# Optimization experiments

Measured on AMD Instinct MI355X. Metric: run time of the kernel, lower is better.

## Reference

```python
import jax, jax.numpy as jnp
from jax import lax
import numpy as np

# ITA requantization params (from init_kwargs)
MQ, SQ = 16384, 8
MK, SK = 16384, 8
MV, SV = 16384, 8
MA, SA = 5, 12
MAV, SAV = 1, 8
MO, SO = 256, 7
NUM_HEADS = 6


def requantize(x, mult, shift, add=0):
    # x * mult, floor-div by 2**shift, add, clamp to int8 range (values kept in float32)
    return jnp.clip(jnp.floor(x * mult / (2.0 ** shift)) + add, -128.0, 127.0)


def ita_softmax(x):
    # x: [B, h, S, Skv] float32 with integer values in [-128, 127]
    B, h, S, Skv = x.shape
    width, bits = 16, 8
    eps_max = 32.0 * bits / (2 ** bits)  # range_scale * bits / 2**bits = 1.0
    groups = Skv // width
    x3 = x.reshape(B * h, S, Skv).astype(jnp.int32)
    # [groups, BH, S, width] for streaming scan over key chunks
    chunks = x3.reshape(B * h, S, groups, width).transpose(2, 0, 1, 3)

    def step(carry, chunk):
        exp_partial_sum, global_max = carry
        current_max = chunk.max(axis=-1)
        update = current_max > global_max
        max_shift = jnp.floor((current_max - global_max).astype(jnp.float32) * eps_max + 0.5).astype(jnp.int32)
        shift_sum = jnp.where(update, max_shift, 0)
        global_max = jnp.where(update, current_max, global_max)
        diff = global_max[..., None] - chunk  # >= 0
        shift = jnp.floor(diff.astype(jnp.float32) * eps_max + 0.5).astype(jnp.int32)
        # 2**bits >> shift  (256 >> shift; any shift >= 9 yields 0, clamp to keep shift defined)
        exp_sum = jnp.sum(jnp.right_shift(jnp.int32(256), jnp.minimum(shift, 31)), axis=-1).astype(jnp.int32)
        exp_partial_sum = jnp.right_shift(exp_partial_sum, jnp.minimum(shift_sum, 31)) + exp_sum
        return (exp_partial_sum, global_max), None

    init = (jnp.zeros((B * h, S), jnp.int32), jnp.full((B * h, S), -128, jnp.int32))
    (exp_partial_sum, global_max), _ = lax.scan(step, init, chunks)

    # (2**bits - 1) * 2**bits = 65280
    inv = jnp.floor(65280.0 / exp_partial_sum.astype(jnp.float32)).astype(jnp.int32)
    diff = global_max[..., None] - x3  # >= 0
    shift = jnp.floor(diff.astype(jnp.float32) * eps_max + 0.5).astype(jnp.int32)
    res = jnp.right_shift(inv[..., None], jnp.minimum(shift, 31)).astype(jnp.uint8)
    return res.reshape(B, h, S, Skv)


def setup_inputs() -> dict:
    key = jax.random.key(0)
    ks = jax.random.split(key, 9)
    B, N, D = 4, 2048, 384
    scale = 1.0 / np.sqrt(D)
    return {
        "x": jax.random.normal(ks[0], (B, N, D), jnp.float32),
        "wq": jax.random.normal(ks[1], (D, D), jnp.float32) * scale,
        "bq": jnp.zeros((D,), jnp.float32),
        "wk": jax.random.normal(ks[2], (D, D), jnp.float32) * scale,
        "bk": jnp.zeros((D,), jnp.float32),
        "wv": jax.random.normal(ks[3], (D, D), jnp.float32) * scale,
        "bv": jnp.zeros((D,), jnp.float32),
        "wo": jax.random.normal(ks[4], (D, D), jnp.float32) * scale,
        "bo": jnp.zeros((D,), jnp.float32),
        "H": 64,
        "W": 32,
    }


def reference(x, wq, bq, wk, bk, wv, bv, wo, bo, H, W):
    B, N, _ = x.shape
    h = NUM_HEADS
    hd = wq.shape[0] // h

    Q = requantize(x @ wq.T + bq, MQ, SQ)
    K = requantize(x @ wk.T + bk, MK, SK)
    V = requantize(x @ wv.T + bv, MV, SV)

    Qr = Q.reshape(B, N, h, hd).transpose(0, 2, 1, 3)  # [B,h,N,hd]
    Kr = K.reshape(B, N, h, hd).transpose(0, 2, 1, 3)
    Vr = V.reshape(B, N, h, hd).transpose(0, 2, 1, 3)

    logits = requantize(jnp.einsum('bhqd,bhkd->bhqk', Qr, Kr), MA, SA)
    attn = ita_softmax(logits)  # uint8 [B,h,N,N]
    ctx = requantize(jnp.einsum('bhqk,bhkd->bhqd', attn.astype(jnp.float32), Vr), MAV, SAV)
    ctx = ctx.transpose(0, 2, 1, 3).reshape(B, N, h * hd)
    out = requantize(ctx @ wo.T + bo, MO, SO)
    return out
```

## Files before the change

kernel.cpp:

```cpp
#include <hip/hip_runtime.h>
#include <stdint.h>

#define NB 4
#define NN 2048
#define ND 384
#define NH 6
#define HD 64
#define ROWS (NB * NN)

typedef int v4i __attribute__((ext_vector_type(4)));
typedef float v4f __attribute__((ext_vector_type(4)));
typedef float v2f __attribute__((ext_vector_type(2)));
typedef _Float16 half_t;
typedef half_t v8h __attribute__((ext_vector_type(8)));

#define PK_FMA_LO(accv, ap, bp)                                            \
    asm("v_pk_fma_f32 %0, %1, %2, %0 op_sel:[0,0,0] op_sel_hi:[0,1,1]"     \
        : "+v"(accv) : "v"(ap), "v"(bp))
#define PK_FMA_HI(accv, ap, bp)                                            \
    asm("v_pk_fma_f32 %0, %1, %2, %0 op_sel:[1,0,0] op_sel_hi:[1,1,1]"     \
        : "+v"(accv) : "v"(ap), "v"(bp))

__global__ __launch_bounds__(256, 3) void qkv_gemm_kernel(
    const float* __restrict__ X,
    const float* __restrict__ Wq, const float* __restrict__ Wk, const float* __restrict__ Wv,
    const float* __restrict__ Bq, const float* __restrict__ Bk, const float* __restrict__ Bv,
    int8_t* __restrict__ Q8, int8_t* __restrict__ K8, int8_t* __restrict__ V8T,
    int* __restrict__ CS)
{
    __shared__ __attribute__((aligned(16))) float As[2][16][132];
    __shared__ __attribute__((aligned(16))) float Bs[2][16][100];
    __shared__ int lcol[96];

    const int t = threadIdx.x;
    const int tx = t & 15;
    const int ty = t >> 4;
    const int row0 = blockIdx.x * 128;
    const int m = blockIdx.y >> 2;
    const int cl0 = (blockIdx.y & 3) * 96;
    const float* W = (m == 0) ? Wq : (m == 1) ? Wk : Wv;
    const float* Bi = (m == 0) ? Bq : (m == 1) ? Bk : Bv;

    const int sr = t >> 1;
    const int sk = (t & 1) * 8;
    const float* xp = X + (size_t)(row0 + sr) * ND + sk;
    const float* wp = W + (size_t)(cl0 + sr) * ND + sk;

    v2f acc[8][3];
#pragma unroll
    for (int i = 0; i < 8; ++i)
#pragma unroll
        for (int p = 0; p < 3; ++p) acc[i][p] = (v2f)0.0f;

    float4 xa0 = *(const float4*)xp;
    float4 xa1 = *(const float4*)(xp + 4);
    float4 wb0, wb1;
    if (t < 192) { wb0 = *(const float4*)wp; wb1 = *(const float4*)(wp + 4); }

    int cur = 0;
    for (int k0 = 0; k0 < ND; k0 += 16) {
        As[cur][sk + 0][sr] = xa0.x; As[cur][sk + 1][sr] = xa0.y;
        As[cur][sk + 2][sr] = xa0.z; As[cur][sk + 3][sr] = xa0.w;
        As[cur][sk + 4][sr] = xa1.x; As[cur][sk + 5][sr] = xa1.y;
        As[cur][sk + 6][sr] = xa1.z; As[cur][sk + 7][sr] = xa1.w;
        if (t < 192) {
            Bs[cur][sk + 0][sr] = wb0.x; Bs[cur][sk + 1][sr] = wb0.y;
            Bs[cur][sk + 2][sr] = wb0.z; Bs[cur][sk + 3][sr] = wb0.w;
            Bs[cur][sk + 4][sr] = wb1.x; Bs[cur][sk + 5][sr] = wb1.y;
            Bs[cur][sk + 6][sr] = wb1.z; Bs[cur][sk + 7][sr] = wb1.w;
        }

        if (k0 + 16 < ND) {
            xa0 = *(const float4*)(xp + k0 + 16);
            xa1 = *(const float4*)(xp + k0 + 20);
            if (t < 192) {
                wb0 = *(const float4*)(wp + k0 + 16);
                wb1 = *(const float4*)(wp + k0 + 20);
            }
        }
        __syncthreads();

#pragma unroll
        for (int kk = 0; kk < 16; ++kk) {
            const v2f* arp  = (const v2f*)&As[cur][kk][ty * 8];
            const v2f* brp  = (const v2f*)&Bs[cur][kk][tx * 4];
            const v2f* brp2 = (const v2f*)&Bs[cur][kk][64 + tx * 2];
            v2f ap0 = arp[0], ap1 = arp[1], ap2 = arp[2], ap3 = arp[3];
            v2f bp0 = brp[0], bp1 = brp[1], bp2 = brp2[0];

            PK_FMA_LO(acc[0][0], ap0, bp0); PK_FMA_LO(acc[0][1], ap0, bp1);
            PK_FMA_LO(acc[0][2], ap0, bp2);
            PK_FMA_HI(acc[1][0], ap0, bp0); PK_FMA_HI(acc[1][1], ap0, bp1);
            PK_FMA_HI(acc[1][2], ap0, bp2);

            PK_FMA_LO(acc[2][0], ap1, bp0); PK_FMA_LO(acc[2][1], ap1, bp1);
            PK_FMA_LO(acc[2][2], ap1, bp2);
            PK_FMA_HI(acc[3][0], ap1, bp0); PK_FMA_HI(acc[3][1], ap1, bp1);
            PK_FMA_HI(acc[3][2], ap1, bp2);

            PK_FMA_LO(acc[4][0], ap2, bp0); PK_FMA_LO(acc[4][1], ap2, bp1);
            PK_FMA_LO(acc[4][2], ap2, bp2);
            PK_FMA_HI(acc[5][0], ap2, bp0); PK_FMA_HI(acc[5][1], ap2, bp1);
            PK_FMA_HI(acc[5][2], ap2, bp2);

            PK_FMA_LO(acc[6][0], ap3, bp0); PK_FMA_LO(acc[6][1], ap3, bp1);
            PK_FMA_LO(acc[6][2], ap3, bp2);
            PK_FMA_HI(acc[7][0], ap3, bp0); PK_FMA_HI(acc[7][1], ap3, bp1);
            PK_FMA_HI(acc[7][2], ap3, bp2);
        }
        cur ^= 1;
    }

    const int bidx = row0 >> 11;
    const int n0 = row0 & 2047;
    const int c1 = cl0 + tx * 4;
    const int c2 = cl0 + 64 + tx * 2;
    const int h1 = c1 >> 6, d1 = c1 & 63;
    const int h2 = c2 >> 6, d2 = c2 & 63;

    if (m != 2) {
        int8_t* Out = (m == 0) ? Q8 : K8;
        const float b1a = Bi[c1], b1b = Bi[c1 + 1], b1c = Bi[c1 + 2], b1d = Bi[c1 + 3];
        const float b2a = Bi[c2], b2b = Bi[c2 + 1];
#pragma unroll
        for (int i = 0; i < 8; ++i) {
            const int n = n0 + ty * 8 + i;
            float v0 = acc[i][0][0] + b1a, v1 = acc[i][0][1] + b1b;
            float v2 = acc[i][1][0] + b1c, v3 = acc[i][1][1] + b1d;
            int q0 = max(-128, min(127, (int)floorf(v0 * 64.0f)));
            int q1 = max(-128, min(127, (int)floorf(v1 * 64.0f)));
            int q2 = max(-128, min(127, (int)floorf(v2 * 64.0f)));
            int q3 = max(-128, min(127, (int)floorf(v3 * 64.0f)));
            uint32_t w = (uint32_t)(q0 & 255) | ((uint32_t)(q1 & 255) << 8)
                       | ((uint32_t)(q2 & 255) << 16) | ((uint32_t)(q3 & 255) << 24);
            *(uint32_t*)(Out + (((size_t)(bidx * NH + h1) * NN) + n) * HD + d1) = w;

            float v4 = acc[i][2][0] + b2a, v5 = acc[i][2][1] + b2b;
            int q4 = max(-128, min(127, (int)floorf(v4 * 64.0f)));
            int q5 = max(-128, min(127, (int)floorf(v5 * 64.0f)));
            *(uint16_t*)(Out + (((size_t)(bidx * NH + h2) * NN) + n) * HD + d2) =
                (uint16_t)((q4 & 255) | ((q5 & 255) << 8));
        }
    } else {
        if (t < 96) lcol[t] = 0;
        __syncthreads();
#pragma unroll
        for (int j = 0; j < 6; ++j) {
            const int lc = (j < 4) ? (tx * 4 + j) : (64 + tx * 2 + (j - 4));
            const int col = cl0 + lc;
            const int head = col >> 6, d = col & 63;
            const float bias = Bi[col];
            int s = 0;
            uint32_t w[2] = {0u, 0u};
#pragma unroll
            for (int i = 0; i < 8; ++i) {
                float v = ((j < 4) ? acc[i][j >> 1][j & 1] : acc[i][2][j - 4]) + bias;
                int qv = (int)floorf(v * 64.0f);
                qv = max(-128, min(127, qv));
                s += qv;
                w[i >> 2] |= (uint32_t)(qv & 255) << (8 * (i & 3));
            }
            uint32_t* dst = (uint32_t*)(V8T + ((size_t)(bidx * NH + head) * HD + d) * NN
                                        + n0 + ty * 8);
            dst[0] = w[0];
            dst[1] = w[1];
            atomicAdd(&lcol[lc], s);
        }
        __syncthreads();
        if (t < 96) {
            const int col = cl0 + t;
            atomicAdd(&CS[(bidx * NH + (col >> 6)) * 64 + (col & 63)], lcol[t]);
        }
    }
}

__global__ __launch_bounds__(256, 4) void attn_kernel(
    const int8_t* __restrict__ Q8, const int8_t* __restrict__ K8,
    const int8_t* __restrict__ V8T, const int* __restrict__ colsum,
    int8_t* __restrict__ CTX8)
{
    __shared__ int Lp[128 * 68];
    __shared__ int gmaxw[128 * 4];
    __shared__ int esumw[128 * 8];

    const int t = threadIdx.x;
    const int wid = t >> 6;
    const int lane = t & 63;
    const int quad = lane >> 4;
    const int l15 = lane & 15;
    const int bh = blockIdx.y;
    const int q0 = blockIdx.x * 16;
    const size_t base = (size_t)bh * NN * HD;
    const v4i zero = {0, 0, 0, 0};

    v4i afrag = *(const v4i*)(Q8 + base + (size_t)(q0 + l15) * HD + quad * 16);
    {
        const int8_t* kp = K8 + base + (size_t)(wid * 32 * 16 + l15) * HD + quad * 16;
        v4i bfrag = *(const v4i*)kp;
        for (int kt = wid * 32; kt < wid * 32 + 32; ++kt) {
            v4i cur = bfrag;
            kp += 16 * HD;
            bfrag = *(const v4i*)kp;
            v4i d = __builtin_amdgcn_mfma_i32_16x16x64_i8(afrag, cur, zero, 0, 0, 0);
            int e[4];
#pragma unroll
            for (int r = 0; r < 4; ++r) {
                int lg = (d[r] * 5) >> 12;
                e[r] = min(127, max(-128, lg));
            }
            int p01 = __builtin_amdgcn_perm(e[1], e[0], 0x00000400);
            int p23 = __builtin_amdgcn_perm(e[3], e[2], 0x00000400);
            Lp[kt * 68 + quad * 16 + l15] = __builtin_amdgcn_perm(p23, p01, 0x05040100);
        }
    }
    __syncthreads();

    int wb[2][16];
#pragma unroll
    for (int it = 0; it < 2; ++it) {
        const int task = t + it * 256;
        const int g = task & 127, qq = task >> 7;
        const int* p = &Lp[g * 68 + qq * 16];
#pragma unroll
        for (int a = 0; a < 4; ++a) {
            v4i v = *(const v4i*)&p[a * 4];
            wb[it][a * 4 + 0] = v.x; wb[it][a * 4 + 1] = v.y;
            wb[it][a * 4 + 2] = v.z; wb[it][a * 4 + 3] = v.w;
        }
        int mx[4];
#pragma unroll
        for (int b = 0; b < 4; ++b) {
            int m = INT_MIN;
#pragma unroll
            for (int j = 0; j < 16; ++j)
                m = max(m, (int)((unsigned)wb[it][j] << (8 * (3 - b))));
            mx[b] = m;
        }
        int p01 = __builtin_amdgcn_perm(mx[1], mx[0], 0x00000703);
        int p23 = __builtin_amdgcn_perm(mx[3], mx[2], 0x00000703);
        gmaxw[g * 4 + qq] = __builtin_amdgcn_perm(p23, p01, 0x05040100);
    }
    __syncthreads();

    if (t < 16) {
        const int wq = t >> 2, bq = 8 * (t & 3);
        int8_t* gb = (int8_t*)gmaxw;
        int m = -128;
        for (int g = 0; g < 128; ++g) {
            int x = (int)(int8_t)(gmaxw[g * 4 + wq] >> bq);
            m = max(m, x);
            gb[g * 16 + t] = (int8_t)m;
        }
    }
    __syncthreads();

#pragma unroll
    for (int it = 0; it < 2; ++it) {
        const int task = t + it * 256;
        const int g = task & 127, qq = task >> 7;
        const int pw = gmaxw[g * 4 + qq];
        uint32_t sp[2] = {0u, 0u};
#pragma unroll
        for (int b = 0; b < 4; ++b) {
            const int M = (int)(int8_t)(pw >> (8 * b));
            const int cb = 8 - M;
            int s = 0;
#pragma unroll
            for (int j = 0; j < 16; ++j) {
                int x = (int)(int8_t)(wb[it][j] >> (8 * b));
                int tt = x + cb;
                s += (tt >= 0) ? (1 << tt) : 0;
            }
            sp[b >> 1] |= (uint32_t)s << (16 * (b & 1));
        }
        *(int2*)&esumw[g * 8 + qq * 2] = make_int2((int)sp[0], (int)sp[1]);
    }
    __syncthreads();

    if (t < 16) {
        const int8_t* gb = (const int8_t*)gmaxw;
        const uint16_t* eb = (const uint16_t*)esumw;
        int E = 0, Mp = -128;
        for (int g = 0; g < 128; ++g) {
            int m = (int)gb[g * 16 + t];
            int d = m - Mp; if (d > 31) d = 31;
            E = (E >> d) + (int)eb[g * 16 + t];
            Mp = m;
        }
        Lp[t * 68 + 64] = 65280 / E;
        Lp[t * 68 + 65] = Mp;
    }
    __syncthreads();

    const int inv_l = Lp[l15 * 68 + 64];
    const int c24 = 24 - Lp[l15 * 68 + 65];
    const int sh8 = 8 * (l15 & 3);
    v4i accs[4] = {zero, zero, zero, zero};
    const int8_t* vtb = V8T + base;

    v4i bf[4];
    {
        const int koff0 = wid * 8 * 64 + quad * 16;
#pragma unroll
        for (int dtb = 0; dtb < 4; ++dtb)
            bf[dtb] = *(const v4i*)(vtb + (size_t)(dtb * 16 + l15) * NN + koff0);
    }
    for (int kc = wid * 8; kc < wid * 8 + 8; ++kc) {
        const int* lp = &Lp[(kc * 4 + quad) * 68 + (l15 >> 2) * 16];
        v4i w4[4];
#pragma unroll
        for (int r = 0; r < 4; ++r) w4[r] = *(const v4i*)&lp[4 * r];

        v4i b0 = bf[0], b1 = bf[1], b2 = bf[2], b3 = bf[3];
        const int koffn = (kc + 1) * 64 + quad * 16;
#pragma unroll
        for (int dtb = 0; dtb < 4; ++dtb)
            bf[dtb] = *(const v4i*)(vtb + (size_t)(dtb * 16 + l15) * NN + koffn);

        v4i a;
#pragma unroll
        for (int r = 0; r < 4; ++r) {
            int u[4];
#pragma unroll
            for (int c = 0; c < 4; ++c) {
                int x = (int)(int8_t)(w4[r][c] >> sh8);
                int t1 = x + c24;
                t1 = (t1 < 0) ? 0 : t1;
                u[c] = (int)((unsigned)inv_l << t1);
            }
            int p01 = __builtin_amdgcn_perm(u[1], u[0], 0x00000703);
            int p23 = __builtin_amdgcn_perm(u[3], u[2], 0x00000703);
            a[r] = __builtin_amdgcn_perm(p23, p01, 0x05040100) ^ (int)0x80808080u;
        }
        accs[0] = __builtin_amdgcn_mfma_i32_16x16x64_i8(a, b0, accs[0], 0, 0, 0);
        accs[1] = __builtin_amdgcn_mfma_i32_16x16x64_i8(a, b1, accs[1], 0, 0, 0);
        accs[2] = __builtin_amdgcn_mfma_i32_16x16x64_i8(a, b2, accs[2], 0, 0, 0);
        accs[3] = __builtin_amdgcn_mfma_i32_16x16x64_i8(a, b3, accs[3], 0, 0, 0);
    }
    __syncthreads();

    if (wid > 0) {
#pragma unroll
        for (int dt = 0; dt < 4; ++dt)
#pragma unroll
            for (int r = 0; r < 4; ++r)
                Lp[(dt * 4 + r) * 192 + (wid - 1) * 64 + lane] = accs[dt][r];
    }
    __syncthreads();
    if (wid == 0) {
        const int bb = bh / NH, hh = bh % NH;
        const int* cs = &colsum[bh * 64];
#pragma unroll
        for (int dt = 0; dt < 4; ++dt) {
            const int dcol = dt * 16 + l15;
            const int corr = cs[dcol] << 7;
#pragma unroll
            for (int r = 0; r < 4; ++r) {
                const int i = dt * 4 + r;
                int val = accs[dt][r]
                        + Lp[i * 192 + 0 * 64 + lane]
                        + Lp[i * 192 + 1 * 64 + lane]
                        + Lp[i * 192 + 2 * 64 + lane];
                const int q = q0 + quad * 4 + r;
                val = (val + corr) >> 8;
                val = min(127, max(-128, val));
                CTX8[((size_t)(bb * NN + q)) * ND + hh * HD + dcol] = (int8_t)val;
            }
        }
    }
}

__global__ __launch_bounds__(384) void wo_convert_kernel(
    const float* __restrict__ Wo, half_t* __restrict__ WoHp, half_t* __restrict__ WoLp)
{
    const int col = blockIdx.x;
    const int k = threadIdx.x;
    float x = Wo[(size_t)col * ND + k];
    half_t h = (half_t)x;
    const size_t d = ((size_t)(k >> 3) * ND + col) * 8 + (k & 7);
    WoHp[d] = h;
    WoLp[d] = (half_t)((x - (float)h) * 2048.0f);
}

__global__ __launch_bounds__(256) void out_gemm_kernel(
    const int8_t* __restrict__ CTX8, const half_t* __restrict__ WoHp,
    const half_t* __restrict__ WoLp, const float* __restrict__ Bo,
    float* __restrict__ out)
{
    __shared__ __attribute__((aligned(16))) int8_t Asl[64 * 400];

    const int t = threadIdx.x;
    const int wid = t >> 6;
    const int lane = t & 63;
    const int quad = lane >> 4;
    const int l15 = lane & 15;
    const int row0 = blockIdx.x * 64;
    const int c0 = blockIdx.y * 64;

#pragma unroll
    for (int pass = 0; pass < 6; ++pass) {
        const int cidx = pass * 256 + t;
        const int row = cidx / 24;
        const int off = (cidx % 24) * 16;
        *(int4*)&Asl[row * 400 + off] =
            *(const int4*)(CTX8 + (size_t)(row0 + row) * ND + off);
    }
    __syncthreads();

    const int8_t* alp = &Asl[(wid * 16 + l15) * 400 + quad * 8];
    const half_t* whp = WoHp + ((size_t)quad * ND + (c0 + l15)) * 8;
    const half_t* wlp = WoLp + ((size_t)quad * ND + (c0 + l15)) * 8;

    v4f accH[4], accL[4];
#pragma unroll
    for (int ct = 0; ct < 4; ct++) { accH[ct] = (v4f)0.0f; accL[ct] = (v4f)0.0f; }

    for (int k0 = 0; k0 < ND; k0 += 32) {
        int2 a8 = *(const int2*)(alp + k0);
        v8h af;
#pragma unroll
        for (int u = 0; u < 4; u++) {
            af[u]     = (half_t)(float)(int)(int8_t)((a8.x >> (8 * u)) & 0xFF);
            af[4 + u] = (half_t)(float)(int)(int8_t)((a8.y >> (8 * u)) & 0xFF);
        }
        const size_t kboff = (size_t)(k0 >> 3) * ND * 8;
#pragma unroll
        for (int ct = 0; ct < 4; ct++) {
            v8h bh8 = *(const v8h*)(whp + kboff + ct * 16 * 8);
            v8h bl8 = *(const v8h*)(wlp + kboff + ct * 16 * 8);
            accH[ct] = __builtin_amdgcn_mfma_f32_16x16x32_f16(af, bh8, accH[ct], 0, 0, 0);
            accL[ct] = __builtin_amdgcn_mfma_f32_16x16x32_f16(af, bl8, accL[ct], 0, 0, 0);
        }
    }

    const float inv2048 = 4.8828125e-4f;
#pragma unroll
    for (int ct = 0; ct < 4; ct++) {
        const int c = c0 + ct * 16 + l15;
        const float bias = Bo[c];
#pragma unroll
        for (int r = 0; r < 4; r++) {
            const int row = row0 + wid * 16 + quad * 4 + r;
            float v = accH[ct][r] + accL[ct][r] * inv2048 + bias;
            float rq = floorf(v * 2.0f);
            rq = fminf(fmaxf(rq, -128.0f), 127.0f);
            out[(size_t)row * ND + c] = rq;
        }
    }
}

extern "C" void kernel_launch(void* const* d_in, const int* in_sizes, int n_in,
                              void* d_out, int out_size, void* d_ws, size_t ws_size,
                              hipStream_t stream)
{
    const float* x  = (const float*)d_in[0];
    const float* wq = (const float*)d_in[1];
    const float* bq = (const float*)d_in[2];
    const float* wk = (const float*)d_in[3];
    const float* bk = (const float*)d_in[4];
    const float* wv = (const float*)d_in[5];
    const float* bv = (const float*)d_in[6];
    const float* wo = (const float*)d_in[7];
    const float* bo = (const float*)d_in[8];
    float* out = (float*)d_out;

    const size_t MAT = (size_t)ROWS * ND;
    int8_t* Q8  = (int8_t*)d_ws;
    int8_t* K8  = Q8 + MAT;
    int8_t* V8T = K8 + MAT;
    int8_t* C8  = V8T + MAT;
    int*    CS  = (int*)(C8 + MAT);
    half_t* WoHp = (half_t*)(CS + NB * NH * 64);
    half_t* WoLp = WoHp + (size_t)ND * ND;

    hipMemsetAsync(CS, 0, (size_t)NB * NH * 64 * sizeof(int), stream);
    wo_convert_kernel<<<dim3(ND), 384, 0, stream>>>(wo, WoHp, WoLp);
    qkv_gemm_kernel<<<dim3(ROWS / 128, 12), 256, 0, stream>>>(
        x, wq, wk, wv, bq, bk, bv, Q8, K8, V8T, CS);
    attn_kernel<<<dim3(NN / 16, NB * NH), 256, 0, stream>>>(Q8, K8, V8T, CS, C8);
    out_gemm_kernel<<<dim3(ROWS / 64, ND / 64), 256, 0, stream>>>(C8, WoHp, WoLp, bo, out);
}
```

Baseline: 273.2 us.

## Parallelize softmax running-max scan and vectorize exp-sum reduction in attention kernel

Replaces the serial 128-step running-max scan done by 16 threads with a block-wide parallel scan: each thread handles 8 groups, then a 16-lane shuffle prefix-max combines them. Partial exp-sums are stored transposed so the remaining serial reduction can read them as vector loads, unrolled by 8. The QK^T loop also prefetches K fragments two tiles ahead instead of one. The aim is to shorten the serialized LDS-bound sections inside the fused attention kernel, at the cost of an extra barrier and a few more registers.

```diff
diff --git a/kernel.cpp b/kernel.cpp
--- a/kernel.cpp
+++ b/kernel.cpp
@@ -196,12 +196,14 @@
     v4i afrag = *(const v4i*)(Q8 + base + (size_t)(q0 + l15) * HD + quad * 16);
     {
         const int8_t* kp = K8 + base + (size_t)(wid * 32 * 16 + l15) * HD + quad * 16;
-        v4i bfrag = *(const v4i*)kp;
+        v4i bf0 = *(const v4i*)kp;
+        v4i bf1 = *(const v4i*)(kp + 16 * HD);
         for (int kt = wid * 32; kt < wid * 32 + 32; ++kt) {
-            v4i cur = bfrag;
+            v4i curk = bf0;
+            bf0 = bf1;
             kp += 16 * HD;
-            bfrag = *(const v4i*)kp;
-            v4i d = __builtin_amdgcn_mfma_i32_16x16x64_i8(afrag, cur, zero, 0, 0, 0);
+            bf1 = *(const v4i*)(kp + 16 * HD);
+            v4i d = __builtin_amdgcn_mfma_i32_16x16x64_i8(afrag, curk, zero, 0, 0, 0);
             int e[4];
 #pragma unroll
             for (int r = 0; r < 4; ++r) {
@@ -242,50 +244,77 @@
     }
     __syncthreads();
 
+    {
+        const int q = t >> 4, c = t & 15;
+        const int wq = q >> 2, bq = 8 * (q & 3);
+        const int gbase = c * 8;
+        int pm[8];
+        int m = -128;
+#pragma unroll
+        for (int i = 0; i < 8; ++i) {
+            int x = (int)(int8_t)(gmaxw[(gbase + i) * 4 + wq] >> bq);
+            m = max(m, x);
+            pm[i] = m;
+        }
+        int incl = m;
+#pragma unroll
+        for (int dl = 1; dl < 16; dl <<= 1) {
+            int v = __shfl_up(incl, dl, 16);
+            if (c >= dl) incl = max(incl, v);
+        }
+        int excl = __shfl_up(incl, 1, 16);
+        if (c == 0) excl = -128;
+        int8_t* gb = (int8_t*)gmaxw;
+#pragma unroll
+        for (int i = 0; i < 8; ++i)
+            gb[(gbase + i) * 16 + q] = (int8_t)max(excl, pm[i]);
+    }
+    __syncthreads();
+
+    {
+        uint16_t* esT = (uint16_t*)esumw;
+#pragma unroll
+        for (int it = 0; it < 2; ++it) {
+            const int task = t + it * 256;
+            const int g = task & 127, qq = task >> 7;
+            const int pw = gmaxw[g * 4 + qq];
+#pragma unroll
+            for (int b = 0; b < 4; ++b) {
+                const int M = (int)(int8_t)(pw >> (8 * b));
+                const int cb = 8 - M;
+                int s = 0;
+#pragma unroll
+                for (int j = 0; j < 16; ++j) {
+                    int x = (int)(int8_t)(wb[it][j] >> (8 * b));
+                    int tt = x + cb;
+                    s += (tt >= 0) ? (1 << tt) : 0;
+                }
+                esT[(qq * 4 + b) * 128 + g] = (uint16_t)s;
+            }
+        }
+    }
+    __syncthreads();
+
     if (t < 16) {
         const int wq = t >> 2, bq = 8 * (t & 3);
-        int8_t* gb = (int8_t*)gmaxw;
-        int m = -128;
-        for (int g = 0; g < 128; ++g) {
-            int x = (int)(int8_t)(gmaxw[g * 4 + wq] >> bq);
-            m = max(m, x);
-            gb[g * 16 + t] = (int8_t)m;
-        }
-    }
-    __syncthreads();
-
-#pragma unroll
-    for (int it = 0; it < 2; ++it) {
-        const int task = t + it * 256;
-        const int g = task & 127, qq = task >> 7;
-        const int pw = gmaxw[g * 4 + qq];
-        uint32_t sp[2] = {0u, 0u};
-#pragma unroll
-        for (int b = 0; b < 4; ++b) {
-            const int M = (int)(int8_t)(pw >> (8 * b));
-            const int cb = 8 - M;
-            int s = 0;
-#pragma unroll
-            for (int j = 0; j < 16; ++j) {
-                int x = (int)(int8_t)(wb[it][j] >> (8 * b));
-                int tt = x + cb;
-                s += (tt >= 0) ? (1 << tt) : 0;
-            }
-            sp[b >> 1] |= (uint32_t)s << (16 * (b & 1));
-        }
-        *(int2*)&esumw[g * 8 + qq * 2] = make_int2((int)sp[0], (int)sp[1]);
-    }
-    __syncthreads();
-
-    if (t < 16) {
-        const int8_t* gb = (const int8_t*)gmaxw;
-        const uint16_t* eb = (const uint16_t*)esumw;
+        const uint16_t* esT = (const uint16_t*)esumw;
         int E = 0, Mp = -128;
-        for (int g = 0; g < 128; ++g) {
-            int m = (int)gb[g * 16 + t];
-            int d = m - Mp; if (d > 31) d = 31;
-            E = (E >> d) + (int)eb[g * 16 + t];
-            Mp = m;
+#pragma unroll 4
+        for (int g0 = 0; g0 < 128; g0 += 8) {
+            int mw[8];
+#pragma unroll
+            for (int i = 0; i < 8; ++i) mw[i] = gmaxw[(g0 + i) * 4 + wq];
+            int4 ev = *(const int4*)&esT[t * 128 + g0];
+            unsigned ew[4] = {(unsigned)ev.x, (unsigned)ev.y,
+                              (unsigned)ev.z, (unsigned)ev.w};
+#pragma unroll
+            for (int i = 0; i < 8; ++i) {
+                int m = (int)(int8_t)(mw[i] >> bq);
+                int d = m - Mp; if (d > 31) d = 31;
+                int e = (int)((ew[i >> 1] >> (16 * (i & 1))) & 0xFFFF);
+                E = (E >> d) + e;
+                Mp = m;
+            }
         }
         Lp[t * 68 + 64] = 65280 / E;
         Lp[t * 68 + 65] = Mp;
```

After: 262.3 us. 1.04x faster.
